# Optimization experiments

Hardware: AMD Instinct MI355X
Metric: run time of the kernel (lower is better)

Reference implementation:

```python
import jax, jax.numpy as jnp
import numpy as np

N_NODES = 50000
N_EDGES = 800000
NUM_FEATURES = 128
HIDDEN = 128
EMBED = 64
OUT_DIM = 1


def setup_inputs() -> dict:
    key = jax.random.key(0)
    ks = jax.random.split(key, 12)
    x = jax.random.normal(ks[0], (N_NODES, NUM_FEATURES), dtype=jnp.float32)
    edge_index = jax.random.randint(ks[1], (2, N_EDGES), 0, N_NODES, dtype=jnp.int64)

    def glorot(k, fan_in, fan_out):
        s = jnp.sqrt(6.0 / (fan_in + fan_out)).astype(jnp.float32)
        return jax.random.uniform(k, (fan_in, fan_out), jnp.float32, -s, s)

    return {
        "x": x,
        "edge_index": edge_index,
        "W1": glorot(ks[2], NUM_FEATURES, HIDDEN),
        "b1": jnp.zeros((HIDDEN,), jnp.float32),
        "Wh": glorot(ks[3], HIDDEN, HIDDEN),
        "bh": jnp.zeros((HIDDEN,), jnp.float32),
        "W2": glorot(ks[4], HIDDEN, EMBED),
        "b2": jnp.zeros((EMBED,), jnp.float32),
        "Wout": glorot(ks[5], EMBED, OUT_DIM),
        "bout": jnp.zeros((OUT_DIM,), jnp.float32),
    }


def _gcn_norm(edge_index, num_nodes):
    # Add self-loops, compute symmetric normalization deg^{-1/2} A_hat deg^{-1/2}
    loop = jnp.arange(num_nodes, dtype=edge_index.dtype)
    src = jnp.concatenate([edge_index[0], loop])
    dst = jnp.concatenate([edge_index[1], loop])
    deg = jax.ops.segment_sum(jnp.ones_like(dst, dtype=jnp.float32), dst,
                              num_segments=num_nodes)
    dis = jnp.where(deg > 0, jax.lax.rsqrt(jnp.maximum(deg, 1.0)), 0.0)
    norm = dis[src] * dis[dst]  # [E+N]
    return src, dst, norm


def _gcn_conv(h, W, b, src, dst, norm, num_nodes):
    h = h @ W  # linear transform first (PyG GCNConv)
    msg = h[src] * norm[:, None]  # gather + scale
    return jax.ops.segment_sum(msg, dst, num_segments=num_nodes) + b


def reference(x, edge_index, W1, b1, Wh, bh, W2, b2, Wout, bout):
    n = x.shape[0]
    src, dst, norm = _gcn_norm(edge_index, n)
    h = jax.nn.relu(_gcn_conv(x, W1, b1, src, dst, norm, n))  # dropout p=0 -> identity
    h = jax.nn.relu(_gcn_conv(h, Wh, bh, src, dst, norm, n))
    h = _gcn_conv(h, W2, b2, src, dst, norm, n)
    out = h @ Wout + bout
    return (out, h)
```

## Files before the change

### kernel.cpp

```cpp
#include <hip/hip_runtime.h>
#include <hip/hip_bf16.h>


#define N_NODES 50000
#define N_EDGES 800000
#define NBUCK 196
#define GB 196
#define EPB 4096

typedef __attribute__((ext_vector_type(8))) short short8;
typedef __attribute__((ext_vector_type(4))) float f32x4;

static __device__ __forceinline__ unsigned short f2bf(float f) {
    __hip_bfloat16 h = __float2bfloat16(f);
    return *reinterpret_cast<unsigned short*>(&h);
}
static __device__ __forceinline__ float bf2f(unsigned short u) {
    return __uint_as_float(((unsigned)u) << 16);
}


__global__ __launch_bounds__(256) void hist_kernel(const int* __restrict__ dstv,
                                                   int* __restrict__ H, int nE) {
    __shared__ int h[NBUCK];
    for (int i = threadIdx.x; i < NBUCK; i += 256) h[i] = 0;
    __syncthreads();
    int base = blockIdx.x * EPB;
#pragma unroll
    for (int i = 0; i < EPB / 256; ++i) {
        int e = base + i * 256 + threadIdx.x;
        if (e < nE) atomicAdd(&h[dstv[e] >> 8], 1);
    }
    __syncthreads();
    for (int i = threadIdx.x; i < NBUCK; i += 256)
        H[i * GB + blockIdx.x] = h[i];
}

__global__ __launch_bounds__(256) void scan1_kernel(int* __restrict__ H,
                                                    int* __restrict__ bsum) {
    __shared__ int s[256];
    int t = threadIdx.x;
    int k = blockIdx.x;
    int v = (t < GB) ? H[k * GB + t] : 0;
    s[t] = v;
    __syncthreads();
    for (int off = 1; off < 256; off <<= 1) {
        int u = (t >= off) ? s[t - off] : 0;
        __syncthreads();
        s[t] += u;
        __syncthreads();
    }
    if (t < GB) H[k * GB + t] = s[t] - v;
    if (t == 255) bsum[k] = s[255];
}

__global__ __launch_bounds__(256) void scan2_kernel(const int* __restrict__ bsum,
                                                    int* __restrict__ bstart,
                                                    int* __restrict__ rowoff_last) {
    __shared__ int s[256];
    int t = threadIdx.x;
    int v = (t < NBUCK) ? bsum[t] : 0;
    s[t] = v;
    __syncthreads();
    for (int off = 1; off < 256; off <<= 1) {
        int u = (t >= off) ? s[t - off] : 0;
        __syncthreads();
        s[t] += u;
        __syncthreads();
    }
    if (t < NBUCK) bstart[t] = s[t] - v;
    if (t == 0) {
        bstart[NBUCK] = N_EDGES;
        *rowoff_last = N_EDGES;
    }
}

__global__ __launch_bounds__(256) void partition_kernel(const int* __restrict__ srcv,
                                                        const int* __restrict__ dstv,
                                                        const int* __restrict__ H,
                                                        const int* __restrict__ bstart,
                                                        int2* __restrict__ P, int nE) {
    __shared__ int cur[NBUCK];
    for (int i = threadIdx.x; i < NBUCK; i += 256)
        cur[i] = bstart[i] + H[i * GB + blockIdx.x];
    __syncthreads();
    int base = blockIdx.x * EPB;
#pragma unroll
    for (int i = 0; i < EPB / 256; ++i) {
        int e = base + i * 256 + threadIdx.x;
        if (e < nE) {
            int d = dstv[e];
            int sv = srcv[e];
            int pos = atomicAdd(&cur[d >> 8], 1);
            P[pos] = make_int2(sv, d);
        }
    }
}

__global__ __launch_bounds__(256) void bucket_csr_kernel(const int2* __restrict__ P,
                                                         const int* __restrict__ bstart,
                                                         int* __restrict__ rowoff,
                                                         float* __restrict__ dis,
                                                         int* __restrict__ csr_src, int n) {
    __shared__ int cnt[256];
    __shared__ int s[256];
    __shared__ int cur[256];
    int t = threadIdx.x;
    int k = blockIdx.x;
    int ebeg = bstart[k], eend = bstart[k + 1];
    cnt[t] = 0;
    __syncthreads();
    for (int e = ebeg + t; e < eend; e += 256)
        atomicAdd(&cnt[P[e].y & 255], 1);
    __syncthreads();
    int myc = cnt[t];
    s[t] = myc;
    __syncthreads();
    for (int off = 1; off < 256; off <<= 1) {
        int v = (t >= off) ? s[t - off] : 0;
        __syncthreads();
        s[t] += v;
        __syncthreads();
    }
    int excl = s[t] - myc;
    int node = (k << 8) + t;
    if (node < n) {
        rowoff[node] = ebeg + excl;
        dis[node] = rsqrtf((float)(myc + 1));
    }
    cur[t] = ebeg + excl;
    __syncthreads();
    for (int e = ebeg + t; e < eend; e += 256) {
        int2 p = P[e];
        int pos = atomicAdd(&cur[p.y & 255], 1);
        csr_src[pos] = p.x;
    }
}

__global__ __launch_bounds__(256) void wprep_all_kernel(
    const float* __restrict__ W1, const float* __restrict__ Wh, const float* __restrict__ W2,
    unsigned short* __restrict__ W1hi, unsigned short* __restrict__ W1lo,
    unsigned short* __restrict__ Whhi, unsigned short* __restrict__ Whlo,
    unsigned short* __restrict__ W2hi, unsigned short* __restrict__ W2lo) {
    int t = blockIdx.x * 256 + threadIdx.x;
    const float* W;
    unsigned short *Hi, *Lo;
    int nout, lt;
    if (t < 16384)      { W = W1; Hi = W1hi; Lo = W1lo; nout = 128; lt = t; }
    else if (t < 32768) { W = Wh; Hi = Whhi; Lo = Whlo; nout = 128; lt = t - 16384; }
    else if (t < 40960) { W = W2; Hi = W2hi; Lo = W2lo; nout = 64;  lt = t - 32768; }
    else return;
    int col = lt % nout, k = lt / nout;
    float v = W[lt];
    unsigned short hi = f2bf(v);
    unsigned short lo = f2bf(v - bf2f(hi));
    Hi[(size_t)col * 128 + k] = hi;
    Lo[(size_t)col * 128 + k] = lo;
}

template <int NOUT>
__global__ __launch_bounds__(256) void gemm_mfma_kernel(
    const float* __restrict__ A,
    const unsigned short* __restrict__ Wthi,
    const unsigned short* __restrict__ Wtlo,
    const float* __restrict__ scale,
    unsigned short* __restrict__ C, int M) {
    constexpr int LDK = 136;
    __shared__ unsigned short sAhi[64 * LDK];
    __shared__ unsigned short sAlo[64 * LDK];

    int tid = threadIdx.x;
    int w = tid >> 6, lane = tid & 63;
    int quad = lane >> 4, m = lane & 15;
    int Rbase = blockIdx.x * 64;
    int Cbase = blockIdx.y * 64;
    int r0 = (w & 1) * 32, c0 = (w >> 1) * 32;

    short8 bh[4][2], bl[4][2];
#pragma unroll
    for (int ks = 0; ks < 4; ++ks)
#pragma unroll
        for (int g = 0; g < 2; ++g) {
            size_t off = (size_t)(Cbase + c0 + g * 16 + m) * 128 + ks * 32 + quad * 8;
            bh[ks][g] = *(const short8*)(Wthi + off);
            bl[ks][g] = *(const short8*)(Wtlo + off);
        }

    for (int i = tid; i < 64 * 32; i += 256) {
        int r = i >> 5, c4 = i & 31;
        int row = Rbase + r;
        float4 v = make_float4(0.f, 0.f, 0.f, 0.f);
        if (row < M) v = ((const float4*)(A + (size_t)row * 128))[c4];
        ushort4 hi, lo;
        hi.x = f2bf(v.x); lo.x = f2bf(v.x - bf2f(hi.x));
        hi.y = f2bf(v.y); lo.y = f2bf(v.y - bf2f(hi.y));
        hi.z = f2bf(v.z); lo.z = f2bf(v.z - bf2f(hi.z));
        hi.w = f2bf(v.w); lo.w = f2bf(v.w - bf2f(hi.w));
        *(ushort4*)(sAhi + r * LDK + c4 * 4) = hi;
        *(ushort4*)(sAlo + r * LDK + c4 * 4) = lo;
    }
    __syncthreads();

    f32x4 z = {0.f, 0.f, 0.f, 0.f};
    f32x4 acc00 = z, acc01 = z, acc10 = z, acc11 = z;

#pragma unroll
    for (int ks = 0; ks < 4; ++ks) {
        int kof = ks * 32 + quad * 8;
        short8 ah0 = *(const short8*)(sAhi + (r0 + m) * LDK + kof);
        short8 ah1 = *(const short8*)(sAhi + (r0 + 16 + m) * LDK + kof);
        short8 al0 = *(const short8*)(sAlo + (r0 + m) * LDK + kof);
        short8 al1 = *(const short8*)(sAlo + (r0 + 16 + m) * LDK + kof);
        acc00 = __builtin_amdgcn_mfma_f32_16x16x32_bf16(ah0, bh[ks][0], acc00, 0, 0, 0);
        acc01 = __builtin_amdgcn_mfma_f32_16x16x32_bf16(ah0, bh[ks][1], acc01, 0, 0, 0);
        acc10 = __builtin_amdgcn_mfma_f32_16x16x32_bf16(ah1, bh[ks][0], acc10, 0, 0, 0);
        acc11 = __builtin_amdgcn_mfma_f32_16x16x32_bf16(ah1, bh[ks][1], acc11, 0, 0, 0);
        acc00 = __builtin_amdgcn_mfma_f32_16x16x32_bf16(ah0, bl[ks][0], acc00, 0, 0, 0);
        acc01 = __builtin_amdgcn_mfma_f32_16x16x32_bf16(ah0, bl[ks][1], acc01, 0, 0, 0);
        acc10 = __builtin_amdgcn_mfma_f32_16x16x32_bf16(ah1, bl[ks][0], acc10, 0, 0, 0);
        acc11 = __builtin_amdgcn_mfma_f32_16x16x32_bf16(ah1, bl[ks][1], acc11, 0, 0, 0);
        acc00 = __builtin_amdgcn_mfma_f32_16x16x32_bf16(al0, bh[ks][0], acc00, 0, 0, 0);
        acc01 = __builtin_amdgcn_mfma_f32_16x16x32_bf16(al0, bh[ks][1], acc01, 0, 0, 0);
        acc10 = __builtin_amdgcn_mfma_f32_16x16x32_bf16(al1, bh[ks][0], acc10, 0, 0, 0);
        acc11 = __builtin_amdgcn_mfma_f32_16x16x32_bf16(al1, bh[ks][1], acc11, 0, 0, 0);
    }

#pragma unroll
    for (int reg = 0; reg < 4; ++reg) {
        int row0g = Rbase + r0 + quad * 4 + reg;
        if (row0g < M) {
            float sc = scale[row0g];
            C[(size_t)row0g * NOUT + Cbase + c0 + m]      = f2bf(acc00[reg] * sc);
            C[(size_t)row0g * NOUT + Cbase + c0 + 16 + m] = f2bf(acc01[reg] * sc);
        }
        int row1g = row0g + 16;
        if (row1g < M) {
            float sc = scale[row1g];
            C[(size_t)row1g * NOUT + Cbase + c0 + m]      = f2bf(acc10[reg] * sc);
            C[(size_t)row1g * NOUT + Cbase + c0 + 16 + m] = f2bf(acc11[reg] * sc);
        }
    }
}

__global__ __launch_bounds__(256) void aggregate128_kernel(
    const int* __restrict__ rowoff, const int* __restrict__ csr_src,
    const float* __restrict__ dis, const unsigned short* __restrict__ tp,
    const float* __restrict__ bias, float* __restrict__ hout, int n) {
    int wid = (blockIdx.x * 256 + threadIdx.x) >> 6;
    int lane = threadIdx.x & 63;
    int h = lane >> 5, lc = lane & 31;
    int n0 = wid * 2;
    if (n0 >= n) return;
    int n1 = n0 + 1;
    bool has1 = (n1 < n);

    float a0[4] = {0.f, 0.f, 0.f, 0.f};
    float a1[4] = {0.f, 0.f, 0.f, 0.f};

#define ROW128(node) (*((const ushort4*)(tp + (size_t)(node) * 128) + lc))
#define ACC(a, u) { a[0] += bf2f(u.x); a[1] += bf2f(u.y); a[2] += bf2f(u.z); a[3] += bf2f(u.w); }

    if (h == 0) { ushort4 u = ROW128(n0); ACC(a0, u); }
    else if (has1) { ushort4 u = ROW128(n1); ACC(a1, u); }

    int mid = rowoff[n0 + 1];
    int i0 = rowoff[n0] + h;
    int i1 = mid + h;
    int end1 = has1 ? rowoff[n1 + 1] : mid;

    while (i0 + 2 < mid && i1 + 2 < end1) {
        int s0a = csr_src[i0], s0b = csr_src[i0 + 2];
        int s1a = csr_src[i1], s1b = csr_src[i1 + 2];
        ushort4 u0 = ROW128(s0a), u1 = ROW128(s0b);
        ushort4 v0 = ROW128(s1a), v1 = ROW128(s1b);
        ACC(a0, u0); ACC(a0, u1);
        ACC(a1, v0); ACC(a1, v1);
        i0 += 4; i1 += 4;
    }
    for (; i0 < mid; i0 += 2) { ushort4 u = ROW128(csr_src[i0]); ACC(a0, u); }
    for (; i1 < end1; i1 += 2) { ushort4 v = ROW128(csr_src[i1]); ACC(a1, v); }
#undef ROW128

#pragma unroll
    for (int j = 0; j < 4; ++j) {
        a0[j] += __shfl_xor(a0[j], 32);
        a1[j] += __shfl_xor(a1[j], 32);
    }

    float4 b = ((const float4*)bias)[lc];
    if (h == 0) {
        float dd = dis[n0];
        float4 r;
        r.x = fmaxf(a0[0] * dd + b.x, 0.f);
        r.y = fmaxf(a0[1] * dd + b.y, 0.f);
        r.z = fmaxf(a0[2] * dd + b.z, 0.f);
        r.w = fmaxf(a0[3] * dd + b.w, 0.f);
        ((float4*)(hout + (size_t)n0 * 128))[lc] = r;
    } else if (has1) {
        float dd = dis[n1];
        float4 r;
        r.x = fmaxf(a1[0] * dd + b.x, 0.f);
        r.y = fmaxf(a1[1] * dd + b.y, 0.f);
        r.z = fmaxf(a1[2] * dd + b.z, 0.f);
        r.w = fmaxf(a1[3] * dd + b.w, 0.f);
        ((float4*)(hout + (size_t)n1 * 128))[lc] = r;
    }
}

__global__ __launch_bounds__(256) void aggregate64_head_kernel(
    const int* __restrict__ rowoff, const int* __restrict__ csr_src,
    const float* __restrict__ dis, const unsigned short* __restrict__ tp,
    const float* __restrict__ bias, const float* __restrict__ Wout,
    const float* __restrict__ bout, float* __restrict__ hout,
    float* __restrict__ out, int n) {
    int wid = (blockIdx.x * 256 + threadIdx.x) >> 6;
    int lane = threadIdx.x & 63;
    int h = lane >> 5, lc = lane & 31;
    int n0 = wid * 2;
    if (n0 >= n) return;
    int n1 = n0 + 1;
    bool has1 = (n1 < n);

    float a0[2] = {0.f, 0.f};
    float a1[2] = {0.f, 0.f};

#define ROW64(node) (*((const ushort2*)(tp + (size_t)(node) * 64) + lc))
#define ACC2(a, u) { a[0] += bf2f(u.x); a[1] += bf2f(u.y); }

    if (h == 0) { ushort2 u = ROW64(n0); ACC2(a0, u); }
    else if (has1) { ushort2 u = ROW64(n1); ACC2(a1, u); }

    int mid = rowoff[n0 + 1];
    int i0 = rowoff[n0] + h;
    int i1 = mid + h;
    int end1 = has1 ? rowoff[n1 + 1] : mid;

    while (i0 + 2 < mid && i1 + 2 < end1) {
        int s0a = csr_src[i0], s0b = csr_src[i0 + 2];
        int s1a = csr_src[i1], s1b = csr_src[i1 + 2];
        ushort2 u0 = ROW64(s0a), u1 = ROW64(s0b);
        ushort2 v0 = ROW64(s1a), v1 = ROW64(s1b);
        ACC2(a0, u0); ACC2(a0, u1);
        ACC2(a1, v0); ACC2(a1, v1);
        i0 += 4; i1 += 4;
    }
    for (; i0 < mid; i0 += 2) { ushort2 u = ROW64(csr_src[i0]); ACC2(a0, u); }
    for (; i1 < end1; i1 += 2) { ushort2 v = ROW64(csr_src[i1]); ACC2(a1, v); }
#undef ROW64

#pragma unroll
    for (int j = 0; j < 2; ++j) {
        a0[j] += __shfl_xor(a0[j], 32);
        a1[j] += __shfl_xor(a1[j], 32);
    }

    int node = h ? n1 : n0;
    float* ap = h ? a1 : a0;
    bool valid = (h == 0) || has1;
    float2 hv = make_float2(0.f, 0.f);
    if (valid) {
        float dd = dis[node];
        float2 b = ((const float2*)bias)[lc];
        hv.x = ap[0] * dd + b.x;
        hv.y = ap[1] * dd + b.y;
        ((float2*)(hout + (size_t)node * 64))[lc] = hv;
    }
    float2 wv = ((const float2*)Wout)[lc];
    float p = valid ? (hv.x * wv.x + hv.y * wv.y) : 0.f;
#pragma unroll
    for (int off = 16; off > 0; off >>= 1) p += __shfl_down(p, off);
    if (lc == 0 && valid) out[node] = p + bout[0];
}

extern "C" void kernel_launch(void* const* d_in, const int* in_sizes, int n_in,
                              void* d_out, int out_size, void* d_ws, size_t ws_size,
                              hipStream_t stream) {
    const float* x    = (const float*)d_in[0];
    const int*   ei   = (const int*)d_in[1];
    const float* W1   = (const float*)d_in[2];
    const float* b1   = (const float*)d_in[3];
    const float* Wh   = (const float*)d_in[4];
    const float* bh   = (const float*)d_in[5];
    const float* W2   = (const float*)d_in[6];
    const float* b2   = (const float*)d_in[7];
    const float* Wout = (const float*)d_in[8];
    const float* bout = (const float*)d_in[9];

    const int N = N_NODES;
    const int E = N_EDGES;
    const int* srcv = ei;
    const int* dstv = ei + E;

    float* out  = (float*)d_out;
    float* hout = (float*)d_out + N;

    char* ws = (char*)d_ws;
    int*   H       = (int*)ws;                          ws += sizeof(int) * NBUCK * GB;
    int*   bsum    = (int*)ws;                          ws += sizeof(int) * NBUCK;
    int*   bstart  = (int*)ws;                          ws += sizeof(int) * (NBUCK + 1);
    int*   rowoff  = (int*)ws;                          ws += sizeof(int) * (N + 1);
    int2*  P       = (int2*)ws;                         ws += sizeof(int2) * E;
    int*   csr_src = (int*)ws;                          ws += sizeof(int) * E;
    float* dis     = (float*)ws;                        ws += sizeof(float) * N;
    unsigned short* W1thi = (unsigned short*)ws;        ws += sizeof(unsigned short) * 128 * 128;
    unsigned short* W1tlo = (unsigned short*)ws;        ws += sizeof(unsigned short) * 128 * 128;
    unsigned short* Whthi = (unsigned short*)ws;        ws += sizeof(unsigned short) * 128 * 128;
    unsigned short* Whtlo = (unsigned short*)ws;        ws += sizeof(unsigned short) * 128 * 128;
    unsigned short* W2thi = (unsigned short*)ws;        ws += sizeof(unsigned short) * 64 * 128;
    unsigned short* W2tlo = (unsigned short*)ws;        ws += sizeof(unsigned short) * 64 * 128;
    unsigned short* bufT  = (unsigned short*)ws;        ws += sizeof(unsigned short) * (size_t)N * 128;
    float* bufH    = (float*)ws;

    wprep_all_kernel<<<160, 256, 0, stream>>>(W1, Wh, W2, W1thi, W1tlo, Whthi, Whtlo, W2thi, W2tlo);

    hist_kernel<<<GB, 256, 0, stream>>>(dstv, H, E);
    scan1_kernel<<<NBUCK, 256, 0, stream>>>(H, bsum);
    scan2_kernel<<<1, 256, 0, stream>>>(bsum, bstart, rowoff + N);
    partition_kernel<<<GB, 256, 0, stream>>>(srcv, dstv, H, bstart, P, E);
    bucket_csr_kernel<<<NBUCK, 256, 0, stream>>>(P, bstart, rowoff, dis, csr_src, N);

    const int aggBlocks = ((N + 1) / 2 * 64 + 255) / 256;
    const int gemmRows = (N + 63) / 64;

    gemm_mfma_kernel<128><<<dim3(gemmRows, 2), 256, 0, stream>>>(x, W1thi, W1tlo, dis, bufT, N);
    aggregate128_kernel<<<aggBlocks, 256, 0, stream>>>(rowoff, csr_src, dis, bufT, b1, bufH, N);

    gemm_mfma_kernel<128><<<dim3(gemmRows, 2), 256, 0, stream>>>(bufH, Whthi, Whtlo, dis, bufT, N);
    aggregate128_kernel<<<aggBlocks, 256, 0, stream>>>(rowoff, csr_src, dis, bufT, bh, bufH, N);

    gemm_mfma_kernel<64><<<dim3(gemmRows, 1), 256, 0, stream>>>(bufH, W2thi, W2tlo, dis, bufT, N);
    aggregate64_head_kernel<<<aggBlocks, 256, 0, stream>>>(
        rowoff, csr_src, dis, bufT, b2, Wout, bout, hout, out, N);
}
```

Baseline: 303.2 us.

## Store transformed features in 16-column panels and aggregate per panel

The GEMM epilogue now writes bf16 output in column-panel layout (16 features per panel, all nodes contiguous), and aggregation runs one block per panel, with each wave handling one node and 16 edges in parallel. The aim is for consecutive blocks to gather from a small panel working set (about 1.6 MB) that stays in L2/cache, rather than from full 256-byte rows scattered across the whole feature matrix. In exchange, each panel launch reads the CSR indices again (8x for the 128-wide layers), gathers are only 32 bytes per edge, and the fused output head becomes a separate kernel.

```diff
diff --git a/kernel.cpp b/kernel.cpp
--- a/kernel.cpp
+++ b/kernel.cpp
@@ -225,151 +225,85 @@
         acc11 = __builtin_amdgcn_mfma_f32_16x16x32_bf16(al1, bh[ks][1], acc11, 0, 0, 0);
     }
 
+    unsigned short* pan0 = C + (size_t)((Cbase + c0) >> 4) * M * 16;
+    unsigned short* pan1 = C + (size_t)((Cbase + c0 + 16) >> 4) * M * 16;
 #pragma unroll
     for (int reg = 0; reg < 4; ++reg) {
         int row0g = Rbase + r0 + quad * 4 + reg;
         if (row0g < M) {
             float sc = scale[row0g];
-            C[(size_t)row0g * NOUT + Cbase + c0 + m]      = f2bf(acc00[reg] * sc);
-            C[(size_t)row0g * NOUT + Cbase + c0 + 16 + m] = f2bf(acc01[reg] * sc);
+            pan0[(size_t)row0g * 16 + m] = f2bf(acc00[reg] * sc);
+            pan1[(size_t)row0g * 16 + m] = f2bf(acc01[reg] * sc);
         }
         int row1g = row0g + 16;
         if (row1g < M) {
             float sc = scale[row1g];
-            C[(size_t)row1g * NOUT + Cbase + c0 + m]      = f2bf(acc10[reg] * sc);
-            C[(size_t)row1g * NOUT + Cbase + c0 + 16 + m] = f2bf(acc11[reg] * sc);
-        }
-    }
-}
-
-__global__ __launch_bounds__(256) void aggregate128_kernel(
+            pan0[(size_t)row1g * 16 + m] = f2bf(acc10[reg] * sc);
+            pan1[(size_t)row1g * 16 + m] = f2bf(acc11[reg] * sc);
+        }
+    }
+}
+
+template <int NPANEL, bool RELU>
+__global__ __launch_bounds__(256) void aggregate_panel_kernel(
     const int* __restrict__ rowoff, const int* __restrict__ csr_src,
     const float* __restrict__ dis, const unsigned short* __restrict__ tp,
     const float* __restrict__ bias, float* __restrict__ hout, int n) {
-    int wid = (blockIdx.x * 256 + threadIdx.x) >> 6;
+    constexpr int F = NPANEL * 16;
+    int p = blockIdx.x & (NPANEL - 1);
+    int node = (blockIdx.x / NPANEL) * 4 + (threadIdx.x >> 6);
+    if (node >= n) return;
     int lane = threadIdx.x & 63;
-    int h = lane >> 5, lc = lane & 31;
-    int n0 = wid * 2;
-    if (n0 >= n) return;
-    int n1 = n0 + 1;
-    bool has1 = (n1 < n);
-
-    float a0[4] = {0.f, 0.f, 0.f, 0.f};
-    float a1[4] = {0.f, 0.f, 0.f, 0.f};
-
-#define ROW128(node) (*((const ushort4*)(tp + (size_t)(node) * 128) + lc))
-#define ACC(a, u) { a[0] += bf2f(u.x); a[1] += bf2f(u.y); a[2] += bf2f(u.z); a[3] += bf2f(u.w); }
-
-    if (h == 0) { ushort4 u = ROW128(n0); ACC(a0, u); }
-    else if (has1) { ushort4 u = ROW128(n1); ACC(a1, u); }
-
-    int mid = rowoff[n0 + 1];
-    int i0 = rowoff[n0] + h;
-    int i1 = mid + h;
-    int end1 = has1 ? rowoff[n1 + 1] : mid;
-
-    while (i0 + 2 < mid && i1 + 2 < end1) {
-        int s0a = csr_src[i0], s0b = csr_src[i0 + 2];
-        int s1a = csr_src[i1], s1b = csr_src[i1 + 2];
-        ushort4 u0 = ROW128(s0a), u1 = ROW128(s0b);
-        ushort4 v0 = ROW128(s1a), v1 = ROW128(s1b);
-        ACC(a0, u0); ACC(a0, u1);
-        ACC(a1, v0); ACC(a1, v1);
-        i0 += 4; i1 += 4;
-    }
-    for (; i0 < mid; i0 += 2) { ushort4 u = ROW128(csr_src[i0]); ACC(a0, u); }
-    for (; i1 < end1; i1 += 2) { ushort4 v = ROW128(csr_src[i1]); ACC(a1, v); }
-#undef ROW128
-
-#pragma unroll
-    for (int j = 0; j < 4; ++j) {
-        a0[j] += __shfl_xor(a0[j], 32);
-        a1[j] += __shfl_xor(a1[j], 32);
-    }
-
-    float4 b = ((const float4*)bias)[lc];
-    if (h == 0) {
-        float dd = dis[n0];
+    int eg = lane >> 2;
+    int cg = lane & 3;
+    const unsigned short* panel = tp + (size_t)p * n * 16;
+
+    float ax = 0.f, ay = 0.f, az = 0.f, aw = 0.f;
+    if (eg == 0) {
+        ushort4 u = *((const ushort4*)(panel + (size_t)node * 16) + cg);
+        ax = bf2f(u.x); ay = bf2f(u.y); az = bf2f(u.z); aw = bf2f(u.w);
+    }
+    int beg = rowoff[node], end = rowoff[node + 1];
+    for (int ib = beg; ib < end; ib += 16) {
+        int e = ib + eg;
+        if (e < end) {
+            int s = csr_src[e];
+            ushort4 u = *((const ushort4*)(panel + (size_t)s * 16) + cg);
+            ax += bf2f(u.x); ay += bf2f(u.y); az += bf2f(u.z); aw += bf2f(u.w);
+        }
+    }
+#pragma unroll
+    for (int off = 4; off < 64; off <<= 1) {
+        ax += __shfl_xor(ax, off);
+        ay += __shfl_xor(ay, off);
+        az += __shfl_xor(az, off);
+        aw += __shfl_xor(aw, off);
+    }
+    if (eg == 0) {
+        float dd = dis[node];
+        float4 b = *((const float4*)(bias + p * 16) + cg);
         float4 r;
-        r.x = fmaxf(a0[0] * dd + b.x, 0.f);
-        r.y = fmaxf(a0[1] * dd + b.y, 0.f);
-        r.z = fmaxf(a0[2] * dd + b.z, 0.f);
-        r.w = fmaxf(a0[3] * dd + b.w, 0.f);
-        ((float4*)(hout + (size_t)n0 * 128))[lc] = r;
-    } else if (has1) {
-        float dd = dis[n1];
-        float4 r;
-        r.x = fmaxf(a1[0] * dd + b.x, 0.f);
-        r.y = fmaxf(a1[1] * dd + b.y, 0.f);
-        r.z = fmaxf(a1[2] * dd + b.z, 0.f);
-        r.w = fmaxf(a1[3] * dd + b.w, 0.f);
-        ((float4*)(hout + (size_t)n1 * 128))[lc] = r;
-    }
-}
-
-__global__ __launch_bounds__(256) void aggregate64_head_kernel(
-    const int* __restrict__ rowoff, const int* __restrict__ csr_src,
-    const float* __restrict__ dis, const unsigned short* __restrict__ tp,
-    const float* __restrict__ bias, const float* __restrict__ Wout,
-    const float* __restrict__ bout, float* __restrict__ hout,
-    float* __restrict__ out, int n) {
-    int wid = (blockIdx.x * 256 + threadIdx.x) >> 6;
+        r.x = ax * dd + b.x; r.y = ay * dd + b.y;
+        r.z = az * dd + b.z; r.w = aw * dd + b.w;
+        if (RELU) {
+            r.x = fmaxf(r.x, 0.f); r.y = fmaxf(r.y, 0.f);
+            r.z = fmaxf(r.z, 0.f); r.w = fmaxf(r.w, 0.f);
+        }
+        *((float4*)(hout + (size_t)node * F + p * 16) + cg) = r;
+    }
+}
+
+__global__ __launch_bounds__(256) void head_kernel(const float* __restrict__ h3,
+                                                   const float* __restrict__ Wout,
+                                                   const float* __restrict__ bout,
+                                                   float* __restrict__ out, int n) {
+    int wave = (blockIdx.x * 256 + threadIdx.x) >> 6;
     int lane = threadIdx.x & 63;
-    int h = lane >> 5, lc = lane & 31;
-    int n0 = wid * 2;
-    if (n0 >= n) return;
-    int n1 = n0 + 1;
-    bool has1 = (n1 < n);
-
-    float a0[2] = {0.f, 0.f};
-    float a1[2] = {0.f, 0.f};
-
-#define ROW64(node) (*((const ushort2*)(tp + (size_t)(node) * 64) + lc))
-#define ACC2(a, u) { a[0] += bf2f(u.x); a[1] += bf2f(u.y); }
-
-    if (h == 0) { ushort2 u = ROW64(n0); ACC2(a0, u); }
-    else if (has1) { ushort2 u = ROW64(n1); ACC2(a1, u); }
-
-    int mid = rowoff[n0 + 1];
-    int i0 = rowoff[n0] + h;
-    int i1 = mid + h;
-    int end1 = has1 ? rowoff[n1 + 1] : mid;
-
-    while (i0 + 2 < mid && i1 + 2 < end1) {
-        int s0a = csr_src[i0], s0b = csr_src[i0 + 2];
-        int s1a = csr_src[i1], s1b = csr_src[i1 + 2];
-        ushort2 u0 = ROW64(s0a), u1 = ROW64(s0b);
-        ushort2 v0 = ROW64(s1a), v1 = ROW64(s1b);
-        ACC2(a0, u0); ACC2(a0, u1);
-        ACC2(a1, v0); ACC2(a1, v1);
-        i0 += 4; i1 += 4;
-    }
-    for (; i0 < mid; i0 += 2) { ushort2 u = ROW64(csr_src[i0]); ACC2(a0, u); }
-    for (; i1 < end1; i1 += 2) { ushort2 v = ROW64(csr_src[i1]); ACC2(a1, v); }
-#undef ROW64
-
-#pragma unroll
-    for (int j = 0; j < 2; ++j) {
-        a0[j] += __shfl_xor(a0[j], 32);
-        a1[j] += __shfl_xor(a1[j], 32);
-    }
-
-    int node = h ? n1 : n0;
-    float* ap = h ? a1 : a0;
-    bool valid = (h == 0) || has1;
-    float2 hv = make_float2(0.f, 0.f);
-    if (valid) {
-        float dd = dis[node];
-        float2 b = ((const float2*)bias)[lc];
-        hv.x = ap[0] * dd + b.x;
-        hv.y = ap[1] * dd + b.y;
-        ((float2*)(hout + (size_t)node * 64))[lc] = hv;
-    }
-    float2 wv = ((const float2*)Wout)[lc];
-    float p = valid ? (hv.x * wv.x + hv.y * wv.y) : 0.f;
-#pragma unroll
-    for (int off = 16; off > 0; off >>= 1) p += __shfl_down(p, off);
-    if (lc == 0 && valid) out[node] = p + bout[0];
+    if (wave >= n) return;
+    float v = h3[(size_t)wave * 64 + lane] * Wout[lane];
+#pragma unroll
+    for (int off = 32; off > 0; off >>= 1) v += __shfl_down(v, off);
+    if (lane == 0) out[wave] = v + bout[0];
 }
 
 extern "C" void kernel_launch(void* const* d_in, const int* in_sizes, int n_in,
@@ -419,16 +353,20 @@
     partition_kernel<<<GB, 256, 0, stream>>>(srcv, dstv, H, bstart, P, E);
     bucket_csr_kernel<<<NBUCK, 256, 0, stream>>>(P, bstart, rowoff, dis, csr_src, N);
 
-    const int aggBlocks = ((N + 1) / 2 * 64 + 255) / 256;
+    const int NB4 = (N + 3) / 4;
     const int gemmRows = (N + 63) / 64;
 
     gemm_mfma_kernel<128><<<dim3(gemmRows, 2), 256, 0, stream>>>(x, W1thi, W1tlo, dis, bufT, N);
-    aggregate128_kernel<<<aggBlocks, 256, 0, stream>>>(rowoff, csr_src, dis, bufT, b1, bufH, N);
+    aggregate_panel_kernel<8, true><<<NB4 * 8, 256, 0, stream>>>(
+        rowoff, csr_src, dis, bufT, b1, bufH, N);
 
     gemm_mfma_kernel<128><<<dim3(gemmRows, 2), 256, 0, stream>>>(bufH, Whthi, Whtlo, dis, bufT, N);
-    aggregate128_kernel<<<aggBlocks, 256, 0, stream>>>(rowoff, csr_src, dis, bufT, bh, bufH, N);
+    aggregate_panel_kernel<8, true><<<NB4 * 8, 256, 0, stream>>>(
+        rowoff, csr_src, dis, bufT, bh, bufH, N);
 
     gemm_mfma_kernel<64><<<dim3(gemmRows, 1), 256, 0, stream>>>(bufH, W2thi, W2tlo, dis, bufT, N);
-    aggregate64_head_kernel<<<aggBlocks, 256, 0, stream>>>(
-        rowoff, csr_src, dis, bufT, b2, Wout, bout, hout, out, N);
-}
+    aggregate_panel_kernel<4, false><<<NB4 * 4, 256, 0, stream>>>(
+        rowoff, csr_src, dis, bufT, b2, hout, N);
+
+    head_kernel<<<((size_t)N * 64 + 255) / 256, 256, 0, stream>>>(hout, Wout, bout, out, N);
+}
```

Result: slower. 478.5 us (+57.8%).

## Store GEMM output in 32-column panels and aggregate per panel for cache locality

Applied to the files above, without the earlier changes.

The two 128-wide GCN layers now have the GEMM write its bf16 output as four column panels of 32 features. A new panel-wise aggregation kernel assigns consecutive blocks to the four panels, so each gather pass touches a 3.2 MB working set. That is meant to keep the random neighbor gathers in L2/MALL instead of spreading over the full 12.8 MB table. In exchange, each 64-byte gather is narrower, and the CSR index lists are read four times.

```diff
diff --git a/kernel.cpp b/kernel.cpp
--- a/kernel.cpp
+++ b/kernel.cpp
@@ -158,7 +158,7 @@
     Lo[(size_t)col * 128 + k] = lo;
 }
 
-template <int NOUT>
+template <int NOUT, bool PANEL>
 __global__ __launch_bounds__(256) void gemm_mfma_kernel(
     const float* __restrict__ A,
     const unsigned short* __restrict__ Wthi,
@@ -228,82 +228,85 @@
 #pragma unroll
     for (int reg = 0; reg < 4; ++reg) {
         int row0g = Rbase + r0 + quad * 4 + reg;
-        if (row0g < M) {
-            float sc = scale[row0g];
-            C[(size_t)row0g * NOUT + Cbase + c0 + m]      = f2bf(acc00[reg] * sc);
-            C[(size_t)row0g * NOUT + Cbase + c0 + 16 + m] = f2bf(acc01[reg] * sc);
-        }
         int row1g = row0g + 16;
-        if (row1g < M) {
-            float sc = scale[row1g];
-            C[(size_t)row1g * NOUT + Cbase + c0 + m]      = f2bf(acc10[reg] * sc);
-            C[(size_t)row1g * NOUT + Cbase + c0 + 16 + m] = f2bf(acc11[reg] * sc);
-        }
-    }
-}
-
-__global__ __launch_bounds__(256) void aggregate128_kernel(
+        if (PANEL) {
+            size_t pbase = (size_t)((Cbase + c0) >> 5) * M * 32;
+            if (row0g < M) {
+                float sc = scale[row0g];
+                C[pbase + (size_t)row0g * 32 + m]      = f2bf(acc00[reg] * sc);
+                C[pbase + (size_t)row0g * 32 + 16 + m] = f2bf(acc01[reg] * sc);
+            }
+            if (row1g < M) {
+                float sc = scale[row1g];
+                C[pbase + (size_t)row1g * 32 + m]      = f2bf(acc10[reg] * sc);
+                C[pbase + (size_t)row1g * 32 + 16 + m] = f2bf(acc11[reg] * sc);
+            }
+        } else {
+            if (row0g < M) {
+                float sc = scale[row0g];
+                C[(size_t)row0g * NOUT + Cbase + c0 + m]      = f2bf(acc00[reg] * sc);
+                C[(size_t)row0g * NOUT + Cbase + c0 + 16 + m] = f2bf(acc01[reg] * sc);
+            }
+            if (row1g < M) {
+                float sc = scale[row1g];
+                C[(size_t)row1g * NOUT + Cbase + c0 + m]      = f2bf(acc10[reg] * sc);
+                C[(size_t)row1g * NOUT + Cbase + c0 + 16 + m] = f2bf(acc11[reg] * sc);
+            }
+        }
+    }
+}
+
+__global__ __launch_bounds__(256) void aggregate128_panel_kernel(
     const int* __restrict__ rowoff, const int* __restrict__ csr_src,
     const float* __restrict__ dis, const unsigned short* __restrict__ tp,
     const float* __restrict__ bias, float* __restrict__ hout, int n) {
-    int wid = (blockIdx.x * 256 + threadIdx.x) >> 6;
-    int lane = threadIdx.x & 63;
-    int h = lane >> 5, lc = lane & 31;
-    int n0 = wid * 2;
+    int p = blockIdx.x & 3;
+    int pair = (blockIdx.x >> 2) * 4 + (threadIdx.x >> 6);
+    int n0 = pair * 2;
     if (n0 >= n) return;
     int n1 = n0 + 1;
     bool has1 = (n1 < n);
-
-    float a0[4] = {0.f, 0.f, 0.f, 0.f};
-    float a1[4] = {0.f, 0.f, 0.f, 0.f};
-
-#define ROW128(node) (*((const ushort4*)(tp + (size_t)(node) * 128) + lc))
-#define ACC(a, u) { a[0] += bf2f(u.x); a[1] += bf2f(u.y); a[2] += bf2f(u.z); a[3] += bf2f(u.w); }
-
-    if (h == 0) { ushort4 u = ROW128(n0); ACC(a0, u); }
-    else if (has1) { ushort4 u = ROW128(n1); ACC(a1, u); }
-
-    int mid = rowoff[n0 + 1];
-    int i0 = rowoff[n0] + h;
-    int i1 = mid + h;
-    int end1 = has1 ? rowoff[n1 + 1] : mid;
-
-    while (i0 + 2 < mid && i1 + 2 < end1) {
-        int s0a = csr_src[i0], s0b = csr_src[i0 + 2];
-        int s1a = csr_src[i1], s1b = csr_src[i1 + 2];
-        ushort4 u0 = ROW128(s0a), u1 = ROW128(s0b);
-        ushort4 v0 = ROW128(s1a), v1 = ROW128(s1b);
-        ACC(a0, u0); ACC(a0, u1);
-        ACC(a1, v0); ACC(a1, v1);
-        i0 += 4; i1 += 4;
-    }
-    for (; i0 < mid; i0 += 2) { ushort4 u = ROW128(csr_src[i0]); ACC(a0, u); }
-    for (; i1 < end1; i1 += 2) { ushort4 v = ROW128(csr_src[i1]); ACC(a1, v); }
-#undef ROW128
-
-#pragma unroll
-    for (int j = 0; j < 4; ++j) {
-        a0[j] += __shfl_xor(a0[j], 32);
-        a1[j] += __shfl_xor(a1[j], 32);
-    }
-
-    float4 b = ((const float4*)bias)[lc];
-    if (h == 0) {
-        float dd = dis[n0];
-        float4 r;
-        r.x = fmaxf(a0[0] * dd + b.x, 0.f);
-        r.y = fmaxf(a0[1] * dd + b.y, 0.f);
-        r.z = fmaxf(a0[2] * dd + b.z, 0.f);
-        r.w = fmaxf(a0[3] * dd + b.w, 0.f);
-        ((float4*)(hout + (size_t)n0 * 128))[lc] = r;
-    } else if (has1) {
-        float dd = dis[n1];
-        float4 r;
-        r.x = fmaxf(a1[0] * dd + b.x, 0.f);
-        r.y = fmaxf(a1[1] * dd + b.y, 0.f);
-        r.z = fmaxf(a1[2] * dd + b.z, 0.f);
-        r.w = fmaxf(a1[3] * dd + b.w, 0.f);
-        ((float4*)(hout + (size_t)n1 * 128))[lc] = r;
+    int lane = threadIdx.x & 63;
+    int q = lane >> 4, lc = lane & 15;
+    bool isN1 = (q >= 2);
+    int par = q & 1;
+    const unsigned short* panel = tp + (size_t)p * n * 32;
+
+    int node = isN1 ? n1 : n0;
+    bool active = !isN1 || has1;
+    float ax = 0.f, ay = 0.f;
+
+    if (active) {
+        if (par == 0) {
+            ushort2 u = *((const ushort2*)(panel + (size_t)node * 32) + lc);
+            ax = bf2f(u.x);
+            ay = bf2f(u.y);
+        }
+        int beg = rowoff[node], end = rowoff[node + 1];
+        int i = beg + par;
+        for (; i + 2 < end; i += 4) {
+            int s0 = csr_src[i], s1 = csr_src[i + 2];
+            ushort2 u0 = *((const ushort2*)(panel + (size_t)s0 * 32) + lc);
+            ushort2 u1 = *((const ushort2*)(panel + (size_t)s1 * 32) + lc);
+            ax += bf2f(u0.x) + bf2f(u1.x);
+            ay += bf2f(u0.y) + bf2f(u1.y);
+        }
+        for (; i < end; i += 2) {
+            ushort2 u = *((const ushort2*)(panel + (size_t)csr_src[i] * 32) + lc);
+            ax += bf2f(u.x);
+            ay += bf2f(u.y);
+        }
+    }
+    ax += __shfl_xor(ax, 16);
+    ay += __shfl_xor(ay, 16);
+
+    if (par == 0 && active) {
+        float dd = dis[node];
+        float2 b = *((const float2*)(bias + p * 32) + lc);
+        float2 r;
+        r.x = fmaxf(ax * dd + b.x, 0.f);
+        r.y = fmaxf(ay * dd + b.y, 0.f);
+        *((float2*)(hout + (size_t)node * 128 + p * 32) + lc) = r;
     }
 }
 
@@ -419,16 +422,19 @@
     partition_kernel<<<GB, 256, 0, stream>>>(srcv, dstv, H, bstart, P, E);
     bucket_csr_kernel<<<NBUCK, 256, 0, stream>>>(P, bstart, rowoff, dis, csr_src, N);
 
-    const int aggBlocks = ((N + 1) / 2 * 64 + 255) / 256;
     const int gemmRows = (N + 63) / 64;
-
-    gemm_mfma_kernel<128><<<dim3(gemmRows, 2), 256, 0, stream>>>(x, W1thi, W1tlo, dis, bufT, N);
-    aggregate128_kernel<<<aggBlocks, 256, 0, stream>>>(rowoff, csr_src, dis, bufT, b1, bufH, N);
-
-    gemm_mfma_kernel<128><<<dim3(gemmRows, 2), 256, 0, stream>>>(bufH, Whthi, Whtlo, dis, bufT, N);
-    aggregate128_kernel<<<aggBlocks, 256, 0, stream>>>(rowoff, csr_src, dis, bufT, bh, bufH, N);
-
-    gemm_mfma_kernel<64><<<dim3(gemmRows, 1), 256, 0, stream>>>(bufH, W2thi, W2tlo, dis, bufT, N);
-    aggregate64_head_kernel<<<aggBlocks, 256, 0, stream>>>(
+    const int aggPBlocks = ((N + 7) / 8) * 4;
+    const int agg64Blocks = ((N + 1) / 2 * 64 + 255) / 256;
+
+    gemm_mfma_kernel<128, true><<<dim3(gemmRows, 2), 256, 0, stream>>>(x, W1thi, W1tlo, dis, bufT, N);
+    aggregate128_panel_kernel<<<aggPBlocks, 256, 0, stream>>>(
+        rowoff, csr_src, dis, bufT, b1, bufH, N);
+
+    gemm_mfma_kernel<128, true><<<dim3(gemmRows, 2), 256, 0, stream>>>(bufH, Whthi, Whtlo, dis, bufT, N);
+    aggregate128_panel_kernel<<<aggPBlocks, 256, 0, stream>>>(
+        rowoff, csr_src, dis, bufT, bh, bufH, N);
+
+    gemm_mfma_kernel<64, false><<<dim3(gemmRows, 1), 256, 0, stream>>>(bufH, W2thi, W2tlo, dis, bufT, N);
+    aggregate64_head_kernel<<<agg64Blocks, 256, 0, stream>>>(
         rowoff, csr_src, dis, bufT, b2, Wout, bout, hout, out, N);
 }
```

New measurement: 344.8 us. +13.7%, slower.

## Fuse neighbor aggregation with the next layer's GEMM via LDS staging

Applied to the files above, without the earlier changes.

Replaces the separate aggregate128 kernel and the following GEMM with one kernel. Each block aggregates 64 nodes into LDS as split bf16 hi/lo, then runs the MFMA GEMM against the next weight matrix and writes the dis-scaled bf16 output directly. This removes the fp32 hidden-state round trip through global memory and two kernel launches per layer. In exchange, each block now does a serial gather over 64 nodes before the GEMM, which lowers parallelism and adds LDS pressure, and the irregular aggregation cannot overlap with the MFMA work.

```diff
diff --git a/kernel.cpp b/kernel.cpp
--- a/kernel.cpp
+++ b/kernel.cpp
@@ -203,7 +203,6 @@
 
     f32x4 z = {0.f, 0.f, 0.f, 0.f};
     f32x4 acc00 = z, acc01 = z, acc10 = z, acc11 = z;
-
 #pragma unroll
     for (int ks = 0; ks < 4; ++ks) {
         int kof = ks * 32 + quad * 8;
@@ -224,7 +223,6 @@
         acc10 = __builtin_amdgcn_mfma_f32_16x16x32_bf16(al1, bh[ks][0], acc10, 0, 0, 0);
         acc11 = __builtin_amdgcn_mfma_f32_16x16x32_bf16(al1, bh[ks][1], acc11, 0, 0, 0);
     }
-
 #pragma unroll
     for (int reg = 0; reg < 4; ++reg) {
         int row0g = Rbase + r0 + quad * 4 + reg;
@@ -242,68 +240,133 @@
     }
 }
 
-__global__ __launch_bounds__(256) void aggregate128_kernel(
+template <int NOUT>
+__global__ __launch_bounds__(256) void agg_gemm_kernel(
     const int* __restrict__ rowoff, const int* __restrict__ csr_src,
     const float* __restrict__ dis, const unsigned short* __restrict__ tp,
-    const float* __restrict__ bias, float* __restrict__ hout, int n) {
-    int wid = (blockIdx.x * 256 + threadIdx.x) >> 6;
-    int lane = threadIdx.x & 63;
-    int h = lane >> 5, lc = lane & 31;
-    int n0 = wid * 2;
-    if (n0 >= n) return;
-    int n1 = n0 + 1;
-    bool has1 = (n1 < n);
-
-    float a0[4] = {0.f, 0.f, 0.f, 0.f};
-    float a1[4] = {0.f, 0.f, 0.f, 0.f};
+    const float* __restrict__ bias,
+    const unsigned short* __restrict__ Wthi, const unsigned short* __restrict__ Wtlo,
+    unsigned short* __restrict__ C, int n) {
+    constexpr int LDK = 136;
+    __shared__ unsigned short sAhi[64 * LDK];
+    __shared__ unsigned short sAlo[64 * LDK];
+
+    int tid = threadIdx.x;
+    int w = tid >> 6, lane = tid & 63;
+    int Rbase = blockIdx.x * 64;
+
+    {
+        int h = lane >> 5, lc = lane & 31;
+        float4 b = ((const float4*)bias)[lc];
+        for (int pp = 0; pp < 8; ++pp) {
+            int lr = w * 16 + pp * 2;
+            int n0 = Rbase + lr, n1 = n0 + 1;
+            float a0[4] = {0.f, 0.f, 0.f, 0.f};
+            float a1[4] = {0.f, 0.f, 0.f, 0.f};
 
 #define ROW128(node) (*((const ushort4*)(tp + (size_t)(node) * 128) + lc))
-#define ACC(a, u) { a[0] += bf2f(u.x); a[1] += bf2f(u.y); a[2] += bf2f(u.z); a[3] += bf2f(u.w); }
-
-    if (h == 0) { ushort4 u = ROW128(n0); ACC(a0, u); }
-    else if (has1) { ushort4 u = ROW128(n1); ACC(a1, u); }
-
-    int mid = rowoff[n0 + 1];
-    int i0 = rowoff[n0] + h;
-    int i1 = mid + h;
-    int end1 = has1 ? rowoff[n1 + 1] : mid;
-
-    while (i0 + 2 < mid && i1 + 2 < end1) {
-        int s0a = csr_src[i0], s0b = csr_src[i0 + 2];
-        int s1a = csr_src[i1], s1b = csr_src[i1 + 2];
-        ushort4 u0 = ROW128(s0a), u1 = ROW128(s0b);
-        ushort4 v0 = ROW128(s1a), v1 = ROW128(s1b);
-        ACC(a0, u0); ACC(a0, u1);
-        ACC(a1, v0); ACC(a1, v1);
-        i0 += 4; i1 += 4;
-    }
-    for (; i0 < mid; i0 += 2) { ushort4 u = ROW128(csr_src[i0]); ACC(a0, u); }
-    for (; i1 < end1; i1 += 2) { ushort4 v = ROW128(csr_src[i1]); ACC(a1, v); }
+#define ACC4(a, u) { a[0] += bf2f(u.x); a[1] += bf2f(u.y); a[2] += bf2f(u.z); a[3] += bf2f(u.w); }
+            if (h == 0) { if (n0 < n) { ushort4 u = ROW128(n0); ACC4(a0, u); } }
+            else        { if (n1 < n) { ushort4 u = ROW128(n1); ACC4(a1, u); } }
+
+            int mid = 0, i0 = h, i1 = h, end1 = 0;
+            if (n0 < n) {
+                int beg0 = rowoff[n0];
+                mid = rowoff[n0 + 1];
+                i0 = beg0 + h;
+                i1 = mid + h;
+                end1 = (n1 < n) ? rowoff[n1 + 1] : mid;
+            }
+            while (i0 + 2 < mid && i1 + 2 < end1) {
+                int s0a = csr_src[i0], s0b = csr_src[i0 + 2];
+                int s1a = csr_src[i1], s1b = csr_src[i1 + 2];
+                ushort4 u0 = ROW128(s0a), u1 = ROW128(s0b);
+                ushort4 v0 = ROW128(s1a), v1 = ROW128(s1b);
+                ACC4(a0, u0); ACC4(a0, u1);
+                ACC4(a1, v0); ACC4(a1, v1);
+                i0 += 4; i1 += 4;
+            }
+            for (; i0 < mid; i0 += 2) { ushort4 u = ROW128(csr_src[i0]); ACC4(a0, u); }
+            for (; i1 < end1; i1 += 2) { ushort4 v = ROW128(csr_src[i1]); ACC4(a1, v); }
 #undef ROW128
-
-#pragma unroll
-    for (int j = 0; j < 4; ++j) {
-        a0[j] += __shfl_xor(a0[j], 32);
-        a1[j] += __shfl_xor(a1[j], 32);
-    }
-
-    float4 b = ((const float4*)bias)[lc];
-    if (h == 0) {
-        float dd = dis[n0];
-        float4 r;
-        r.x = fmaxf(a0[0] * dd + b.x, 0.f);
-        r.y = fmaxf(a0[1] * dd + b.y, 0.f);
-        r.z = fmaxf(a0[2] * dd + b.z, 0.f);
-        r.w = fmaxf(a0[3] * dd + b.w, 0.f);
-        ((float4*)(hout + (size_t)n0 * 128))[lc] = r;
-    } else if (has1) {
-        float dd = dis[n1];
-        float4 r;
-        r.x = fmaxf(a1[0] * dd + b.x, 0.f);
-        r.y = fmaxf(a1[1] * dd + b.y, 0.f);
-        r.z = fmaxf(a1[2] * dd + b.z, 0.f);
-        r.w = fmaxf(a1[3] * dd + b.w, 0.f);
-        ((float4*)(hout + (size_t)n1 * 128))[lc] = r;
+#undef ACC4
+#pragma unroll
+            for (int j = 0; j < 4; ++j) {
+                a0[j] += __shfl_xor(a0[j], 32);
+                a1[j] += __shfl_xor(a1[j], 32);
+            }
+            int node = h ? n1 : n0;
+            float* ap = h ? a1 : a0;
+            ushort4 hi = make_ushort4(0, 0, 0, 0), lo = make_ushort4(0, 0, 0, 0);
+            if (node < n) {
+                float dd = dis[node];
+                float rx = fmaxf(ap[0] * dd + b.x, 0.f);
+                float ry = fmaxf(ap[1] * dd + b.y, 0.f);
+                float rz = fmaxf(ap[2] * dd + b.z, 0.f);
+                float rw = fmaxf(ap[3] * dd + b.w, 0.f);
+                hi.x = f2bf(rx); lo.x = f2bf(rx - bf2f(hi.x));
+                hi.y = f2bf(ry); lo.y = f2bf(ry - bf2f(hi.y));
+                hi.z = f2bf(rz); lo.z = f2bf(rz - bf2f(hi.z));
+                hi.w = f2bf(rw); lo.w = f2bf(rw - bf2f(hi.w));
+            }
+            int r = lr + h;
+            *(ushort4*)(sAhi + r * LDK + lc * 4) = hi;
+            *(ushort4*)(sAlo + r * LDK + lc * 4) = lo;
+        }
+    }
+    __syncthreads();
+
+    int quad = (lane >> 4) & 3, m = lane & 15;
+    int r0 = (w & 1) * 32, c0 = (w >> 1) * 32;
+
+#pragma unroll
+    for (int ch = 0; ch < NOUT / 64; ++ch) {
+        short8 bh[4][2], bl[4][2];
+#pragma unroll
+        for (int ks = 0; ks < 4; ++ks)
+#pragma unroll
+            for (int g = 0; g < 2; ++g) {
+                size_t off = (size_t)(ch * 64 + c0 + g * 16 + m) * 128 + ks * 32 + quad * 8;
+                bh[ks][g] = *(const short8*)(Wthi + off);
+                bl[ks][g] = *(const short8*)(Wtlo + off);
+            }
+        f32x4 z = {0.f, 0.f, 0.f, 0.f};
+        f32x4 acc00 = z, acc01 = z, acc10 = z, acc11 = z;
+#pragma unroll
+        for (int ks = 0; ks < 4; ++ks) {
+            int kof = ks * 32 + quad * 8;
+            short8 ah0 = *(const short8*)(sAhi + (r0 + m) * LDK + kof);
+            short8 ah1 = *(const short8*)(sAhi + (r0 + 16 + m) * LDK + kof);
+            short8 al0 = *(const short8*)(sAlo + (r0 + m) * LDK + kof);
+            short8 al1 = *(const short8*)(sAlo + (r0 + 16 + m) * LDK + kof);
+            acc00 = __builtin_amdgcn_mfma_f32_16x16x32_bf16(ah0, bh[ks][0], acc00, 0, 0, 0);
+            acc01 = __builtin_amdgcn_mfma_f32_16x16x32_bf16(ah0, bh[ks][1], acc01, 0, 0, 0);
+            acc10 = __builtin_amdgcn_mfma_f32_16x16x32_bf16(ah1, bh[ks][0], acc10, 0, 0, 0);
+            acc11 = __builtin_amdgcn_mfma_f32_16x16x32_bf16(ah1, bh[ks][1], acc11, 0, 0, 0);
+            acc00 = __builtin_amdgcn_mfma_f32_16x16x32_bf16(ah0, bl[ks][0], acc00, 0, 0, 0);
+            acc01 = __builtin_amdgcn_mfma_f32_16x16x32_bf16(ah0, bl[ks][1], acc01, 0, 0, 0);
+            acc10 = __builtin_amdgcn_mfma_f32_16x16x32_bf16(ah1, bl[ks][0], acc10, 0, 0, 0);
+            acc11 = __builtin_amdgcn_mfma_f32_16x16x32_bf16(ah1, bl[ks][1], acc11, 0, 0, 0);
+            acc00 = __builtin_amdgcn_mfma_f32_16x16x32_bf16(al0, bh[ks][0], acc00, 0, 0, 0);
+            acc01 = __builtin_amdgcn_mfma_f32_16x16x32_bf16(al0, bh[ks][1], acc01, 0, 0, 0);
+            acc10 = __builtin_amdgcn_mfma_f32_16x16x32_bf16(al1, bh[ks][0], acc10, 0, 0, 0);
+            acc11 = __builtin_amdgcn_mfma_f32_16x16x32_bf16(al1, bh[ks][1], acc11, 0, 0, 0);
+        }
+#pragma unroll
+        for (int reg = 0; reg < 4; ++reg) {
+            int row0g = Rbase + r0 + quad * 4 + reg;
+            if (row0g < n) {
+                float sc = dis[row0g];
+                C[(size_t)row0g * NOUT + ch * 64 + c0 + m]      = f2bf(acc00[reg] * sc);
+                C[(size_t)row0g * NOUT + ch * 64 + c0 + 16 + m] = f2bf(acc01[reg] * sc);
+            }
+            int row1g = row0g + 16;
+            if (row1g < n) {
+                float sc = dis[row1g];
+                C[(size_t)row1g * NOUT + ch * 64 + c0 + m]      = f2bf(acc10[reg] * sc);
+                C[(size_t)row1g * NOUT + ch * 64 + c0 + 16 + m] = f2bf(acc11[reg] * sc);
+            }
+        }
     }
 }
 
@@ -347,6 +410,7 @@
     for (; i0 < mid; i0 += 2) { ushort2 u = ROW64(csr_src[i0]); ACC2(a0, u); }
     for (; i1 < end1; i1 += 2) { ushort2 v = ROW64(csr_src[i1]); ACC2(a1, v); }
 #undef ROW64
+#undef ACC2
 
 #pragma unroll
     for (int j = 0; j < 2; ++j) {
@@ -408,8 +472,8 @@
     unsigned short* Whtlo = (unsigned short*)ws;        ws += sizeof(unsigned short) * 128 * 128;
     unsigned short* W2thi = (unsigned short*)ws;        ws += sizeof(unsigned short) * 64 * 128;
     unsigned short* W2tlo = (unsigned short*)ws;        ws += sizeof(unsigned short) * 64 * 128;
-    unsigned short* bufT  = (unsigned short*)ws;        ws += sizeof(unsigned short) * (size_t)N * 128;
-    float* bufH    = (float*)ws;
+    unsigned short* bufT1 = (unsigned short*)ws;        ws += sizeof(unsigned short) * (size_t)N * 128;
+    unsigned short* bufT2 = (unsigned short*)ws;
 
     wprep_all_kernel<<<160, 256, 0, stream>>>(W1, Wh, W2, W1thi, W1tlo, Whthi, Whtlo, W2thi, W2tlo);
 
@@ -419,16 +483,17 @@
     partition_kernel<<<GB, 256, 0, stream>>>(srcv, dstv, H, bstart, P, E);
     bucket_csr_kernel<<<NBUCK, 256, 0, stream>>>(P, bstart, rowoff, dis, csr_src, N);
 
-    const int aggBlocks = ((N + 1) / 2 * 64 + 255) / 256;
     const int gemmRows = (N + 63) / 64;
-
-    gemm_mfma_kernel<128><<<dim3(gemmRows, 2), 256, 0, stream>>>(x, W1thi, W1tlo, dis, bufT, N);
-    aggregate128_kernel<<<aggBlocks, 256, 0, stream>>>(rowoff, csr_src, dis, bufT, b1, bufH, N);
-
-    gemm_mfma_kernel<128><<<dim3(gemmRows, 2), 256, 0, stream>>>(bufH, Whthi, Whtlo, dis, bufT, N);
-    aggregate128_kernel<<<aggBlocks, 256, 0, stream>>>(rowoff, csr_src, dis, bufT, bh, bufH, N);
-
-    gemm_mfma_kernel<64><<<dim3(gemmRows, 1), 256, 0, stream>>>(bufH, W2thi, W2tlo, dis, bufT, N);
-    aggregate64_head_kernel<<<aggBlocks, 256, 0, stream>>>(
-        rowoff, csr_src, dis, bufT, b2, Wout, bout, hout, out, N);
-}
+    const int agg64Blocks = ((N + 1) / 2 * 64 + 255) / 256;
+
+    gemm_mfma_kernel<128><<<dim3(gemmRows, 2), 256, 0, stream>>>(x, W1thi, W1tlo, dis, bufT1, N);
+
+    agg_gemm_kernel<128><<<gemmRows, 256, 0, stream>>>(
+        rowoff, csr_src, dis, bufT1, b1, Whthi, Whtlo, bufT2, N);
+
+    agg_gemm_kernel<64><<<gemmRows, 256, 0, stream>>>(
+        rowoff, csr_src, dis, bufT2, bh, W2thi, W2tlo, bufT1, N);
+
+    aggregate64_head_kernel<<<agg64Blocks, 256, 0, stream>>>(
+        rowoff, csr_src, dis, bufT1, b2, Wout, bout, hout, out, N);
+}
```

New measurement: 366.5 us. 1.21x slower.
